# Kernel tuning notes

Hardware: AMD Instinct MI355X
Metric: run time of the kernel (lower is better)

## Reference

```python
import jax, jax.numpy as jnp
import numpy as np

N = 100000      # nodes
E = 800000      # edges (avg degree 8)
D_IN = 128      # in_channels
HEADS = 8
C = 16          # out_channels per head (heads*C = 128 output dim)
NEG_SLOPE = 0.2  # PyG GATConv default leaky_relu slope


def setup_inputs() -> dict:
    key = jax.random.key(0)
    ks = jax.random.split(key, 12)
    s = 1.0 / np.sqrt(D_IN)
    x = jax.random.normal(ks[0], (N, D_IN), jnp.float32)
    ei = jax.random.randint(ks[1], (2, E), 0, N, jnp.int32)
    return {
        "x": x,
        "ei": ei,
        # conv_in GATConv params
        "W_in": jax.random.normal(ks[2], (D_IN, HEADS * C), jnp.float32) * s,
        "a_src_in": jax.random.normal(ks[3], (HEADS, C), jnp.float32) * s,
        "a_dst_in": jax.random.normal(ks[4], (HEADS, C), jnp.float32) * s,
        "b_in": jnp.zeros((HEADS * C,), jnp.float32),
        # conv_out GATConv params (applied to flipped edges)
        "W_out": jax.random.normal(ks[5], (D_IN, HEADS * C), jnp.float32) * s,
        "a_src_out": jax.random.normal(ks[6], (HEADS, C), jnp.float32) * s,
        "a_dst_out": jax.random.normal(ks[7], (HEADS, C), jnp.float32) * s,
        "b_out": jnp.zeros((HEADS * C,), jnp.float32),
    }


def _gat_conv(x, src, dst, W, a_src, a_dst, b):
    # h: [N, H, C] projected node features
    h = (x @ W).reshape(N, HEADS, C)
    # per-node attention logits [N, H]
    alpha_src = jnp.einsum("nhc,hc->nh", h, a_src)
    alpha_dst = jnp.einsum("nhc,hc->nh", h, a_dst)
    # per-edge logits, message flows src -> dst; softmax grouped by dst
    logits = jax.nn.leaky_relu(alpha_src[src] + alpha_dst[dst], NEG_SLOPE)  # [E, H]
    seg_max = jax.ops.segment_max(logits, dst, num_segments=N)              # [N, H]
    ex = jnp.exp(logits - seg_max[dst])
    denom = jax.ops.segment_sum(ex, dst, num_segments=N)                    # [N, H]
    coef = ex / denom[dst]                                                  # [E, H]
    msg = h[src] * coef[:, :, None]                                         # [E, H, C]
    out = jax.ops.segment_sum(msg, dst, num_segments=N)                     # [N, H, C]
    return out.reshape(N, HEADS * C) + b


def reference(x, ei, W_in, a_src_in, a_dst_in, b_in, W_out, a_src_out, a_dst_out, b_out):
    src, dst = ei[0], ei[1]
    # DirSeq: conv_in on (src->dst), conv_out on flipped edges (dst->src)
    x_in = _gat_conv(x, src, dst, W_in, a_src_in, a_dst_in, b_in)
    x_out = _gat_conv(x, dst, src, W_out, a_src_out, a_dst_out, b_out)
    return x_in + x_out
```

## Files before the change

### kernel.cpp

```cpp
#include <hip/hip_runtime.h>

#define N_NODES 100000
#define N_EDGES 800000
#define NEG 0.2f
#define PB_SHIFT 8
#define PB_NODES 256
#define N_PBKT ((N_NODES + PB_NODES - 1) / PB_NODES)
#define CAP 4096
#define TILE_E 4096
#define EPT 16
#define PART_BLOCKS ((N_EDGES + TILE_E - 1) / TILE_E)
#define GEMM_BLOCKS ((N_NODES + 127) / 128)

typedef __attribute__((ext_vector_type(8))) short bf16x8;
typedef __attribute__((ext_vector_type(4))) float f32x4;

__device__ inline unsigned short f2bf(float f) {
    unsigned u = __float_as_uint(f);
    u += 0x7fffu + ((u >> 16) & 1u);
    return (unsigned short)(u >> 16);
}
__device__ inline float bf2f_lo(unsigned u) { return __uint_as_float(u << 16); }
__device__ inline float bf2f_hi(unsigned u) { return __uint_as_float(u & 0xffff0000u); }

__global__ __launch_bounds__(256) void prep_w_kernel(
    const float* __restrict__ W_in, const float* __restrict__ W_out,
    const float* __restrict__ as_in, const float* __restrict__ ad_in,
    const float* __restrict__ as_out, const float* __restrict__ ad_out,
    unsigned short* __restrict__ Wf, int* __restrict__ gcur,
    int* __restrict__ adj_in, int* __restrict__ adj_out,
    int* __restrict__ offs_in, int* __restrict__ offs_out)
{
    const int t = blockIdx.x * 256 + threadIdx.x;
    if (t < 2 * N_PBKT) gcur[t] = 0;
    if (t < 8) { adj_in[N_EDGES + t] = 0; adj_out[N_EDGES + t] = 0; }
    if (t == 0) { offs_in[N_NODES] = N_EDGES; offs_out[N_NODES] = N_EDGES; }
    if (t >= 2 * 4 * 9 * 64) return;
    const int lane = t & 63;
    const int rest = t >> 6;
    const int ct  = rest % 9;
    const int kb  = (rest / 9) & 3;
    const int dir = rest / 36;
    const float* W  = dir ? W_out  : W_in;
    const float* as = dir ? as_out : as_in;
    const float* ad = dir ? ad_out : ad_in;
    const int m16 = lane & 15, quad = lane >> 4;

    bf16x8 o;
#pragma unroll
    for (int j = 0; j < 8; ++j) {
        const int k = kb * 32 + quad * 8 + j;
        float v;
        if (ct < 8) {
            v = W[k * 128 + ct * 16 + m16];
        } else {
            const float* av = (m16 < 8) ? as : ad;
            const int hh = m16 & 7;
            v = 0.f;
            for (int c = 0; c < 16; ++c)
                v += W[k * 128 + hh * 16 + c] * av[hh * 16 + c];
        }
        o[j] = (short)f2bf(v);
    }
    *(bf16x8*)&Wf[(long long)t * 8] = o;
}

__global__ __launch_bounds__(256) void mega_kernel(
    const float* __restrict__ x,
    const unsigned short* __restrict__ Wf,
    unsigned short* __restrict__ h_in, unsigned short* __restrict__ h_out,
    float* __restrict__ asrc_in, float* __restrict__ adst_in,
    float* __restrict__ asrc_out, float* __restrict__ adst_out,
    const int* __restrict__ ei, int* __restrict__ gcur,
    int* __restrict__ binned0, int* __restrict__ binned1)
{
    const int tid = threadIdx.x;

    if (blockIdx.x < PART_BLOCKS) {
        __shared__ int hist0[N_PBKT];
        __shared__ int curs0[N_PBKT];
        __shared__ int hist1[N_PBKT];
        __shared__ int curs1[N_PBKT];
        for (int i = tid; i < N_PBKT; i += 256) { hist0[i] = 0; hist1[i] = 0; }
        __syncthreads();

        const int e0 = blockIdx.x * TILE_E;
        int sv[EPT], tv[EPT];
#pragma unroll
        for (int i = 0; i < EPT; ++i) {
            const int e = e0 + i * 256 + tid;
            if (e < N_EDGES) {
                sv[i] = ei[e];
                tv[i] = ei[N_EDGES + e];
                atomicAdd(&hist0[tv[i] >> PB_SHIFT], 1);
                atomicAdd(&hist1[sv[i] >> PB_SHIFT], 1);
            } else {
                sv[i] = -1; tv[i] = 0;
            }
        }
        __syncthreads();
        for (int b = tid; b < N_PBKT; b += 256) {
            int c = hist0[b];
            curs0[b] = c ? atomicAdd(&gcur[b], c) : 0;
            c = hist1[b];
            curs1[b] = c ? atomicAdd(&gcur[N_PBKT + b], c) : 0;
        }
        __syncthreads();
#pragma unroll
        for (int i = 0; i < EPT; ++i) {
            if (sv[i] >= 0) {
                const int b0 = tv[i] >> PB_SHIFT;
                int pos = atomicAdd(&curs0[b0], 1);
                if (pos < CAP)
                    binned0[b0 * CAP + pos] = (sv[i] << 8) | (tv[i] & (PB_NODES - 1));
                const int b1 = sv[i] >> PB_SHIFT;
                pos = atomicAdd(&curs1[b1], 1);
                if (pos < CAP)
                    binned1[b1 * CAP + pos] = (tv[i] << 8) | (sv[i] & (PB_NODES - 1));
            }
        }
        return;
    }

    const int gb  = blockIdx.x - PART_BLOCKS;
    const int dir = gb >= GEMM_BLOCKS;
    const int bx  = gb - dir * GEMM_BLOCKS;
    unsigned short* h = dir ? h_out : h_in;
    float* asrc = dir ? asrc_out : asrc_in;
    float* adst = dir ? adst_out : adst_in;

    const int lane = tid & 63;
    const int wave = tid >> 6;
    const int m16  = lane & 15;
    const int quad = lane >> 4;
    const int rbase = bx * 128 + wave * 32;

    f32x4 acc[2][8];
    f32x4 acc_a[2];
#pragma unroll
    for (int rt = 0; rt < 2; ++rt) {
        acc_a[rt] = f32x4{0.f, 0.f, 0.f, 0.f};
#pragma unroll
        for (int ct = 0; ct < 8; ++ct)
            acc[rt][ct] = f32x4{0.f, 0.f, 0.f, 0.f};
    }

    const unsigned short* wf = Wf + (long long)dir * 4 * 9 * 64 * 8;

#pragma unroll
    for (int kb = 0; kb < 4; ++kb) {
        const int k0 = kb * 32 + quad * 8;
        bf16x8 a[2];
#pragma unroll
        for (int rt = 0; rt < 2; ++rt) {
            int r = rbase + rt * 16 + m16;
            r = r < N_NODES ? r : N_NODES - 1;
            const float4 v0 = *(const float4*)&x[(long long)r * 128 + k0];
            const float4 v1 = *(const float4*)&x[(long long)r * 128 + k0 + 4];
            a[rt][0] = (short)f2bf(v0.x); a[rt][1] = (short)f2bf(v0.y);
            a[rt][2] = (short)f2bf(v0.z); a[rt][3] = (short)f2bf(v0.w);
            a[rt][4] = (short)f2bf(v1.x); a[rt][5] = (short)f2bf(v1.y);
            a[rt][6] = (short)f2bf(v1.z); a[rt][7] = (short)f2bf(v1.w);
        }
#pragma unroll
        for (int ct = 0; ct < 9; ++ct) {
            const bf16x8 b = *(const bf16x8*)&wf[(long long)((kb * 9 + ct) * 64 + lane) * 8];
            if (ct < 8) {
                acc[0][ct] = __builtin_amdgcn_mfma_f32_16x16x32_bf16(a[0], b, acc[0][ct], 0, 0, 0);
                acc[1][ct] = __builtin_amdgcn_mfma_f32_16x16x32_bf16(a[1], b, acc[1][ct], 0, 0, 0);
            } else {
                acc_a[0] = __builtin_amdgcn_mfma_f32_16x16x32_bf16(a[0], b, acc_a[0], 0, 0, 0);
                acc_a[1] = __builtin_amdgcn_mfma_f32_16x16x32_bf16(a[1], b, acc_a[1], 0, 0, 0);
            }
        }
    }

#pragma unroll
    for (int rt = 0; rt < 2; ++rt) {
#pragma unroll
        for (int r = 0; r < 4; ++r) {
            const int row = rbase + rt * 16 + quad * 4 + r;
            if (row < N_NODES) {
                unsigned short* hp = &h[(long long)row * 128 + m16];
#pragma unroll
                for (int ct = 0; ct < 8; ++ct)
                    hp[ct * 16] = f2bf(acc[rt][ct][r]);
                const float av = acc_a[rt][r];
                if (m16 < 8) asrc[row * 8 + m16] = av;
                else         adst[row * 8 + (m16 - 8)] = av;
            }
        }
    }
}

__global__ __launch_bounds__(256) void place_kernel(
    const int* __restrict__ binned0, const int* __restrict__ binned1,
    const int* __restrict__ gcur,
    int* __restrict__ adj_in, int* __restrict__ adj_out,
    int* __restrict__ offs_in, int* __restrict__ offs_out)
{
    const int b   = blockIdx.x;
    const int dir = blockIdx.y;
    const int* bp = (dir ? binned1 : binned0) + b * CAP;
    const int* gc = gcur + dir * N_PBKT;
    int* adj  = dir ? adj_out  : adj_in;
    int* offs = dir ? offs_out : offs_in;

    const int base = b << PB_SHIFT;
    const int tid = threadIdx.x;
    const int cntb = min(gc[b], CAP);

    __shared__ int slab[CAP];
    __shared__ int cnt[PB_NODES];
    __shared__ int sc[PB_NODES];
    __shared__ int cur[PB_NODES];
    __shared__ int red[PB_NODES];

    int part = 0;
    for (int j = tid; j < b; j += 256) part += min(gc[j], CAP);
    red[tid] = part;
    cnt[tid] = 0;
    for (int p = tid; p < cntb; p += 256) slab[p] = bp[p];
    __syncthreads();
#pragma unroll
    for (int off = 128; off > 0; off >>= 1) {
        if (tid < off) red[tid] += red[tid + off];
        __syncthreads();
    }
    const int beg = red[0];
    for (int p = tid; p < cntb; p += 256)
        atomicAdd(&cnt[slab[p] & (PB_NODES - 1)], 1);
    __syncthreads();
    const int v = cnt[tid];
    sc[tid] = v;
    __syncthreads();
#pragma unroll
    for (int off = 1; off < PB_NODES; off <<= 1) {
        int t = (tid >= off) ? sc[tid - off] : 0;
        __syncthreads();
        sc[tid] += t;
        __syncthreads();
    }
    const int excl = beg + sc[tid] - v;
    cur[tid] = excl;
    const int node = base + tid;
    if (node < N_NODES) offs[node] = excl;
    __syncthreads();
    for (int p = tid; p < cntb; p += 256) {
        const int pk = slab[p];
        adj[atomicAdd(&cur[pk & (PB_NODES - 1)], 1)] = pk >> 8;
    }
}

__global__ __launch_bounds__(256) void gather_kernel(
    const int* __restrict__ offs_in, const int* __restrict__ adj_in,
    const int* __restrict__ offs_out, const int* __restrict__ adj_out,
    const unsigned short* __restrict__ h_in, const unsigned short* __restrict__ h_out,
    const float* __restrict__ asrc_in, const float* __restrict__ adst_in,
    const float* __restrict__ asrc_out, const float* __restrict__ adst_out,
    const float* __restrict__ b_in, const float* __restrict__ b_out,
    float* __restrict__ out)
{
    int n = (blockIdx.x * 256 + threadIdx.x) >> 6;
    if (n >= N_NODES) return;
    n = __builtin_amdgcn_readfirstlane(n);
    const int lane = threadIdx.x & 63;
    const int c0 = lane * 2;
    const int hh = lane >> 3;
    const int g8 = lane & 7;
    const int grpbase = lane & 56;

    float acc0 = b_in[c0] + b_out[c0];
    float acc1 = b_in[c0 + 1] + b_out[c0 + 1];

#define DIR_BLOCK(OFFS, ADJ, HX, ASRC, ADST)                                   \
    {                                                                          \
        const int beg = OFFS[n], end = OFFS[n + 1];                            \
        if (end > beg) {                                                       \
            const float ad = ADST[n * 8 + hh];                                 \
            float num0 = 0.f, num1 = 0.f, den = 0.f;                           \
            for (int p = beg; p < end; p += 8) {                               \
                const int q = p + g8;                                          \
                const int nbv = ADJ[q];                 \
                float l = ASRC[nbv * 8 + hh] + ad;                             \
                l = l > 0.f ? l : NEG * l;                                     \
                float w = __expf(l);                                           \
                w = (q < end) ? w : 0.f;                                       \
                den += w;                                                      \
                _Pragma("unroll")                                              \
                for (int g = 0; g < 8; ++g) {                                  \
                    const int nb = ADJ[p + g];           \
                    const float w_g = __shfl(w, grpbase + g, 64);              \
                    const unsigned hv = *(const unsigned*)&HX[(long long)nb * 128 + c0]; \
                    num0 += w_g * bf2f_lo(hv);                                 \
                    num1 += w_g * bf2f_hi(hv);                                 \
                }                                                              \
            }                                                                  \
            den += __shfl_xor(den, 1, 64);                                     \
            den += __shfl_xor(den, 2, 64);                                     \
            den += __shfl_xor(den, 4, 64);                                     \
            const float rden = 1.f / den;                                      \
            acc0 += num0 * rden;                                               \
            acc1 += num1 * rden;                                               \
        }                                                                      \
    }

    DIR_BLOCK(offs_in, adj_in, h_in, asrc_in, adst_in)
    DIR_BLOCK(offs_out, adj_out, h_out, asrc_out, adst_out)
#undef DIR_BLOCK

    *(float2*)&out[(long long)n * 128 + c0] = float2{acc0, acc1};
}

extern "C" void kernel_launch(void* const* d_in, const int* in_sizes, int n_in,
                              void* d_out, int out_size, void* d_ws, size_t ws_size,
                              hipStream_t stream) {
    const float* x      = (const float*)d_in[0];
    const int*   ei     = (const int*)  d_in[1];
    const float* W_in   = (const float*)d_in[2];
    const float* as_in  = (const float*)d_in[3];
    const float* ad_in  = (const float*)d_in[4];
    const float* b_in   = (const float*)d_in[5];
    const float* W_out  = (const float*)d_in[6];
    const float* as_out = (const float*)d_in[7];
    const float* ad_out = (const float*)d_in[8];
    const float* b_out  = (const float*)d_in[9];
    float* out = (float*)d_out;

    char* ws = (char*)d_ws;
    const long long NH = (long long)N_NODES * 128;
    unsigned short* h_in  = (unsigned short*)ws;    ws += NH * 2;
    unsigned short* h_out = (unsigned short*)ws;    ws += NH * 2;
    unsigned short* Wf    = (unsigned short*)ws;    ws += 2LL * 4 * 9 * 64 * 8 * 2;
    float* asrc_in   = (float*)ws;                  ws += N_NODES * 8 * 4;
    float* adst_in   = (float*)ws;                  ws += N_NODES * 8 * 4;
    float* asrc_out  = (float*)ws;                  ws += N_NODES * 8 * 4;
    float* adst_out  = (float*)ws;                  ws += N_NODES * 8 * 4;
    int* binned0     = (int*)ws;                    ws += (long long)N_PBKT * CAP * 4;
    int* binned1     = (int*)ws;                    ws += (long long)N_PBKT * CAP * 4;
    int* adj_in      = (int*)ws;                    ws += (N_EDGES + 8) * 4;
    int* adj_out     = (int*)ws;                    ws += (N_EDGES + 8) * 4;
    int* offs_in     = (int*)ws;                    ws += (N_NODES + 1) * 4;
    int* offs_out    = (int*)ws;                    ws += (N_NODES + 1) * 4;
    int* gcur        = (int*)ws;                    ws += 2 * N_PBKT * 4;

    prep_w_kernel<<<(2 * 4 * 9 * 64 + 255) / 256, 256, 0, stream>>>(
        W_in, W_out, as_in, ad_in, as_out, ad_out, Wf, gcur,
        adj_in, adj_out, offs_in, offs_out);

    mega_kernel<<<PART_BLOCKS + 2 * GEMM_BLOCKS, 256, 0, stream>>>(
        x, Wf, h_in, h_out, asrc_in, adst_in, asrc_out, adst_out,
        ei, gcur, binned0, binned1);

    place_kernel<<<dim3(N_PBKT, 2), 256, 0, stream>>>(
        binned0, binned1, gcur, adj_in, adj_out, offs_in, offs_out);

    gather_kernel<<<(N_NODES * 64 + 255) / 256, 256, 0, stream>>>(
        offs_in, adj_in, offs_out, adj_out, h_in, h_out,
        asrc_in, adst_in, asrc_out, adst_out, b_in, b_out, out);
}
```

Measured before the change: 256.0 us.

## Fuse place stage into partition blocks via grid-wide atomic barrier

Removes the separate place_kernel launch. The partition blocks of mega_kernel now wait at a global atomic counter until all partition blocks are done, then each handles up to four bucket/direction slabs to build the CSR offsets and adjacency. This saves one kernel launch and lets placement overlap with the GEMM blocks. It relies on all PART_BLOCKS (about 196) being co-resident, which risks deadlock if they are not, and shared memory is now a single union buffer sized for the larger use.

```diff
diff --git a/kernel.cpp b/kernel.cpp
--- a/kernel.cpp
+++ b/kernel.cpp
@@ -11,6 +11,7 @@
 #define EPT 16
 #define PART_BLOCKS ((N_EDGES + TILE_E - 1) / TILE_E)
 #define GEMM_BLOCKS ((N_NODES + 127) / 128)
+#define SMEM_INTS (CAP + 4 * PB_NODES)
 
 typedef __attribute__((ext_vector_type(8))) short bf16x8;
 typedef __attribute__((ext_vector_type(4))) float f32x4;
@@ -32,7 +33,7 @@
     int* __restrict__ offs_in, int* __restrict__ offs_out)
 {
     const int t = blockIdx.x * 256 + threadIdx.x;
-    if (t < 2 * N_PBKT) gcur[t] = 0;
+    if (t < 2 * N_PBKT + 1) gcur[t] = 0;
     if (t < 8) { adj_in[N_EDGES + t] = 0; adj_out[N_EDGES + t] = 0; }
     if (t == 0) { offs_in[N_NODES] = N_EDGES; offs_out[N_NODES] = N_EDGES; }
     if (t >= 2 * 4 * 9 * 64) return;
@@ -72,15 +73,18 @@
     float* __restrict__ asrc_in, float* __restrict__ adst_in,
     float* __restrict__ asrc_out, float* __restrict__ adst_out,
     const int* __restrict__ ei, int* __restrict__ gcur,
-    int* __restrict__ binned0, int* __restrict__ binned1)
+    int* __restrict__ binned0, int* __restrict__ binned1,
+    int* __restrict__ adj_in, int* __restrict__ adj_out,
+    int* __restrict__ offs_in, int* __restrict__ offs_out)
 {
+    __shared__ int smem[SMEM_INTS];
     const int tid = threadIdx.x;
 
     if (blockIdx.x < PART_BLOCKS) {
-        __shared__ int hist0[N_PBKT];
-        __shared__ int curs0[N_PBKT];
-        __shared__ int hist1[N_PBKT];
-        __shared__ int curs1[N_PBKT];
+        int* hist0 = smem;
+        int* curs0 = smem + N_PBKT;
+        int* hist1 = smem + 2 * N_PBKT;
+        int* curs1 = smem + 3 * N_PBKT;
         for (int i = tid; i < N_PBKT; i += 256) { hist0[i] = 0; hist1[i] = 0; }
         __syncthreads();
 
@@ -119,6 +123,73 @@
                     binned1[b1 * CAP + pos] = (tv[i] << 8) | (sv[i] & (PB_NODES - 1));
             }
         }
+
+        int* flag = gcur + 2 * N_PBKT;
+        __threadfence();
+        __syncthreads();
+        if (tid == 0)
+            __hip_atomic_fetch_add(flag, 1, __ATOMIC_RELEASE, __HIP_MEMORY_SCOPE_AGENT);
+        if (tid == 0) {
+            while (__hip_atomic_load(flag, __ATOMIC_ACQUIRE, __HIP_MEMORY_SCOPE_AGENT) < PART_BLOCKS)
+                __builtin_amdgcn_s_sleep(2);
+        }
+        __syncthreads();
+        __threadfence();
+
+        int* slab = smem;
+        int* cnt  = smem + CAP;
+        int* sc   = cnt + PB_NODES;
+        int* cur  = sc + PB_NODES;
+        int* red  = cur + PB_NODES;
+
+        for (int u = 0; u < 4; ++u) {
+            const int bd = u * PART_BLOCKS + blockIdx.x;
+            if (bd >= 2 * N_PBKT) break;
+            const int dir = bd >= N_PBKT;
+            const int b   = bd - dir * N_PBKT;
+            const int* bp = (dir ? binned1 : binned0) + b * CAP;
+            const int* gc = gcur + dir * N_PBKT;
+            int* adj  = dir ? adj_out  : adj_in;
+            int* offs = dir ? offs_out : offs_in;
+            const int base = b << PB_SHIFT;
+            const int cntb = min(gc[b], CAP);
+
+            __syncthreads();
+            int part = 0;
+            for (int j = tid; j < b; j += 256) part += min(gc[j], CAP);
+            red[tid] = part;
+            cnt[tid] = 0;
+            for (int p = tid; p < cntb; p += 256) slab[p] = bp[p];
+            __syncthreads();
+#pragma unroll
+            for (int off = 128; off > 0; off >>= 1) {
+                if (tid < off) red[tid] += red[tid + off];
+                __syncthreads();
+            }
+            const int beg = red[0];
+            for (int p = tid; p < cntb; p += 256)
+                atomicAdd(&cnt[slab[p] & (PB_NODES - 1)], 1);
+            __syncthreads();
+            const int v = cnt[tid];
+            sc[tid] = v;
+            __syncthreads();
+#pragma unroll
+            for (int off = 1; off < PB_NODES; off <<= 1) {
+                int t2 = (tid >= off) ? sc[tid - off] : 0;
+                __syncthreads();
+                sc[tid] += t2;
+                __syncthreads();
+            }
+            const int excl = beg + sc[tid] - v;
+            cur[tid] = excl;
+            const int node = base + tid;
+            if (node < N_NODES) offs[node] = excl;
+            __syncthreads();
+            for (int p = tid; p < cntb; p += 256) {
+                const int pk = slab[p];
+                adj[atomicAdd(&cur[pk & (PB_NODES - 1)], 1)] = pk >> 8;
+            }
+        }
         return;
     }
 
@@ -190,65 +261,6 @@
                 else         adst[row * 8 + (m16 - 8)] = av;
             }
         }
-    }
-}
-
-__global__ __launch_bounds__(256) void place_kernel(
-    const int* __restrict__ binned0, const int* __restrict__ binned1,
-    const int* __restrict__ gcur,
-    int* __restrict__ adj_in, int* __restrict__ adj_out,
-    int* __restrict__ offs_in, int* __restrict__ offs_out)
-{
-    const int b   = blockIdx.x;
-    const int dir = blockIdx.y;
-    const int* bp = (dir ? binned1 : binned0) + b * CAP;
-    const int* gc = gcur + dir * N_PBKT;
-    int* adj  = dir ? adj_out  : adj_in;
-    int* offs = dir ? offs_out : offs_in;
-
-    const int base = b << PB_SHIFT;
-    const int tid = threadIdx.x;
-    const int cntb = min(gc[b], CAP);
-
-    __shared__ int slab[CAP];
-    __shared__ int cnt[PB_NODES];
-    __shared__ int sc[PB_NODES];
-    __shared__ int cur[PB_NODES];
-    __shared__ int red[PB_NODES];
-
-    int part = 0;
-    for (int j = tid; j < b; j += 256) part += min(gc[j], CAP);
-    red[tid] = part;
-    cnt[tid] = 0;
-    for (int p = tid; p < cntb; p += 256) slab[p] = bp[p];
-    __syncthreads();
-#pragma unroll
-    for (int off = 128; off > 0; off >>= 1) {
-        if (tid < off) red[tid] += red[tid + off];
-        __syncthreads();
-    }
-    const int beg = red[0];
-    for (int p = tid; p < cntb; p += 256)
-        atomicAdd(&cnt[slab[p] & (PB_NODES - 1)], 1);
-    __syncthreads();
-    const int v = cnt[tid];
-    sc[tid] = v;
-    __syncthreads();
-#pragma unroll
-    for (int off = 1; off < PB_NODES; off <<= 1) {
-        int t = (tid >= off) ? sc[tid - off] : 0;
-        __syncthreads();
-        sc[tid] += t;
-        __syncthreads();
-    }
-    const int excl = beg + sc[tid] - v;
-    cur[tid] = excl;
-    const int node = base + tid;
-    if (node < N_NODES) offs[node] = excl;
-    __syncthreads();
-    for (int p = tid; p < cntb; p += 256) {
-        const int pk = slab[p];
-        adj[atomicAdd(&cur[pk & (PB_NODES - 1)], 1)] = pk >> 8;
     }
 }
 
@@ -342,7 +354,7 @@
     int* adj_out     = (int*)ws;                    ws += (N_EDGES + 8) * 4;
     int* offs_in     = (int*)ws;                    ws += (N_NODES + 1) * 4;
     int* offs_out    = (int*)ws;                    ws += (N_NODES + 1) * 4;
-    int* gcur        = (int*)ws;                    ws += 2 * N_PBKT * 4;
+    int* gcur        = (int*)ws;                    ws += (2 * N_PBKT + 1) * 4;
 
     prep_w_kernel<<<(2 * 4 * 9 * 64 + 255) / 256, 256, 0, stream>>>(
         W_in, W_out, as_in, ad_in, as_out, ad_out, Wf, gcur,
@@ -350,10 +362,7 @@
 
     mega_kernel<<<PART_BLOCKS + 2 * GEMM_BLOCKS, 256, 0, stream>>>(
         x, Wf, h_in, h_out, asrc_in, adst_in, asrc_out, adst_out,
-        ei, gcur, binned0, binned1);
-
-    place_kernel<<<dim3(N_PBKT, 2), 256, 0, stream>>>(
-        binned0, binned1, gcur, adj_in, adj_out, offs_in, offs_out);
+        ei, gcur, binned0, binned1, adj_in, adj_out, offs_in, offs_out);
 
     gather_kernel<<<(N_NODES * 64 + 255) / 256, 256, 0, stream>>>(
         offs_in, adj_in, offs_out, adj_out, h_in, h_out,
```

Result: slower. 373.4 us (+45.9%).
